# Performance work log

Hardware: AMD Instinct MI355X
Metric: run time of the kernel (lower is better)

The kernel has to match this reference:

```python
import jax, jax.numpy as jnp
import numpy as np

B, N, DM, DC, TOPK = 1024, 131072, 2048, 64, 16
EPS_RES = 1e-8
EPS_SQRT = 1e-12


def setup_inputs() -> dict:
    key = jax.random.key(0)
    k1, k2, k3, k4, k5 = jax.random.split(key, 5)
    query = jax.random.normal(k1, (B, DM), dtype=jnp.float32)
    stored_coords = jax.random.normal(k2, (N, DC), dtype=jnp.float32)
    resilience = jax.random.uniform(k3, (N,), dtype=jnp.float32)
    W_proj = jax.random.normal(k4, (DM, DC), dtype=jnp.float32) / np.sqrt(DM)
    M = jax.random.normal(k5, (DC, DC), dtype=jnp.float32) / np.sqrt(DC)
    return {"query": query, "stored_coords": stored_coords,
            "resilience": resilience, "W_proj": W_proj, "M": M,
            "top_k": TOPK}


def reference(query, stored_coords, resilience, W_proj, M, top_k):
    # Manifold projection: embeddings -> coordinate chart (B, DC)
    qc = query @ W_proj
    # Learned PSD metric G = M M^T
    G = M @ M.T
    # Geodesic distance d(x,y) = sqrt((x-y)^T G (x-y)), expanded into GEMMs:
    qG = qc @ G                      # (B, DC)
    sG = stored_coords @ G           # (N, DC)
    q2 = jnp.sum(qc * qG, axis=-1)               # (B,)
    s2 = jnp.sum(stored_coords * sG, axis=-1)    # (N,)
    cross = qG @ stored_coords.T                 # (B, N) -- dominant GEMM
    d2 = q2[:, None] + s2[None, :] - 2.0 * cross
    dists = jnp.sqrt(jnp.maximum(d2, 0.0) + EPS_SQRT)
    # LIoR resilience weighting
    dists = dists / (resilience + EPS_RES)[None, :]
    # top-k SMALLEST distances (torch.topk largest=False)
    neg_top, topk_indices = jax.lax.top_k(-dists, top_k)
    return -neg_top, topk_indices
```

## Files before the change

### kernel.cpp

```cpp
#include <hip/hip_runtime.h>
#include <stdint.h>

#define NQ 1024
#define NS 131072
#define DMM 2048
#define DCC 64
#define K_TOP 16
#define EPS_RES_F 1e-8f
#define EPS_SQRT_F 1e-12f
#define EPS_A 0.01f

#define NCH 128
#define CHR (NS / NCH)
#define OVCAP 65536
#define SLOTS 24
#define MTOT (NCH * SLOTS)
#define EPT (MTOT / 256)
#define SCAP 3328

typedef __attribute__((ext_vector_type(8))) short short8v;
typedef __attribute__((ext_vector_type(4))) float f32x4;
typedef unsigned long long u64t;

__device__ __forceinline__ unsigned short f2bf(float x) {
  unsigned u = __float_as_uint(x);
  unsigned r = (u + 0x7FFFu + ((u >> 16) & 1u)) >> 16;
  return (unsigned short)r;
}
__device__ __forceinline__ unsigned bf16_down_pos(float x) {
  return __float_as_uint(x) >> 16;
}
__device__ __forceinline__ unsigned bf16_up_pos(float x) {
  const unsigned u = __float_as_uint(x);
  return (u >> 16) + ((u & 0xFFFFu) ? 1u : 0u);
}

__device__ __forceinline__ void gl_lds16(const void* g, void* l) {
  __builtin_amdgcn_global_load_lds(
      (const __attribute__((address_space(1))) unsigned int*)g,
      (__attribute__((address_space(3))) unsigned int*)l, 16, 0, 0);
}

__device__ __forceinline__ float exact_key(const float* __restrict__ stored,
                                           const float* qgl, float q2v,
                                           const float4* __restrict__ aux4, int n) {
  const float4* srow = reinterpret_cast<const float4*>(stored + (size_t)n * DCC);
  float a = 0.f;
#pragma unroll
  for (int kb = 0; kb < 16; ++kb) {
    const float4 qv = *reinterpret_cast<const float4*>(&qgl[4 * kb]);
    const float4 sv = srow[kb];
    a = fmaf(qv.w, sv.w, fmaf(qv.z, sv.z, fmaf(qv.y, sv.y, fmaf(qv.x, sv.x, a))));
  }
  const float4 av = aux4[n];
  const float d2 = fmaf(-2.f, a, q2v + av.x);
  return (fmaxf(d2, 0.f) + EPS_SQRT_F) * av.w;
}

__device__ __forceinline__ void bin_rank256(const int* hist, int rank, int lane,
                                            int& binOut, int& baseOut, int& totalOut) {
  const int b0 = hist[4 * lane + 0], b1 = hist[4 * lane + 1];
  const int b2 = hist[4 * lane + 2], b3 = hist[4 * lane + 3];
  const int s01 = b0 + b1, s012 = s01 + b2;
  const int s = s012 + b3;
  int inc = s;
#pragma unroll
  for (int off = 1; off < 64; off <<= 1) {
    const int u = __shfl_up(inc, off);
    if (lane >= off) inc += u;
  }
  totalOut = __shfl(inc, 63);
  const int excl = inc - s;
  const bool has = (excl <= rank) && (rank < inc);
  const unsigned long long mask = __ballot(has);
  if (mask == 0ULL) { binOut = -1; baseOut = 0; return; }
  const int who = __ffsll((unsigned long long)mask) - 1;
  const int exclW = __shfl(excl, who);
  const int c0 = __shfl(b0, who);
  const int c01 = __shfl(s01, who);
  const int c012 = __shfl(s012, who);
  const int r = rank - exclW;
  int sub, base;
  if (r < c0) { sub = 0; base = 0; }
  else if (r < c01) { sub = 1; base = c0; }
  else if (r < c012) { sub = 2; base = c01; }
  else { sub = 3; base = c012; }
  binOut = 4 * who + sub;
  baseOut = exclW + base;
}

__global__ __launch_bounds__(256) void g_kernel(const float* __restrict__ M,
                                                float* __restrict__ G) {
  __shared__ __align__(16) float Ml[64 * 66];
  const int t = threadIdx.x;
  for (int p = 0; p < 16; ++p) {
    int i = p * 256 + t;
    Ml[(i >> 6) * 66 + (i & 63)] = M[i];
  }
  __syncthreads();
  const int e = blockIdx.x * 256 + t;
  const int i = e >> 6, j = e & 63;
  float a = 0.f;
#pragma unroll
  for (int k = 0; k < 64; ++k) a = fmaf(Ml[i * 66 + k], Ml[j * 66 + k], a);
  G[e] = a;
}

__global__ __launch_bounds__(256) void q_kernel(
    const float* __restrict__ query, const float* __restrict__ W,
    const float* __restrict__ G, float* __restrict__ qGT,
    float* __restrict__ qGr, unsigned short* __restrict__ qGh,
    float* __restrict__ q2o, float* __restrict__ qeo) {
  __shared__ __align__(16) float qs[4][DMM];
  __shared__ float part[4][4][64];
  __shared__ float qc[4][64];
  const int t = threadIdx.x;
  const int qb = blockIdx.x * 4;
  {
    const float4* src = reinterpret_cast<const float4*>(query + (size_t)qb * DMM);
    float4* dst = reinterpret_cast<float4*>(&qs[0][0]);
#pragma unroll
    for (int r = 0; r < 8; ++r) dst[r * 256 + t] = src[r * 256 + t];
  }
  __syncthreads();
  const int c = t & 63, seg = t >> 6;
  float p0 = 0.f, p1 = 0.f, p2 = 0.f, p3 = 0.f;
  const int kbase = seg * 512;
  for (int ki = 0; ki < 512; ++ki) {
    const int k = kbase + ki;
    const float w = W[(size_t)k * 64 + c];
    p0 = fmaf(qs[0][k], w, p0);
    p1 = fmaf(qs[1][k], w, p1);
    p2 = fmaf(qs[2][k], w, p2);
    p3 = fmaf(qs[3][k], w, p3);
  }
  part[0][seg][c] = p0; part[1][seg][c] = p1;
  part[2][seg][c] = p2; part[3][seg][c] = p3;
  __syncthreads();
  {
    const int q = t >> 6, cc = t & 63;
    qc[q][cc] = part[q][0][cc] + part[q][1][cc] + part[q][2][cc] + part[q][3][cc];
  }
  __syncthreads();
  const int w = t >> 6, lane = t & 63;
  float g = 0.f;
  for (int j = 0; j < 64; ++j) g = fmaf(qc[w][j], G[j * 64 + lane], g);
  const int q = qb + w;
  qGT[(size_t)lane * NQ + q] = g;
  qGr[(size_t)q * DCC + lane] = g;
  qGh[(size_t)q * DCC + lane] = f2bf(g);
  float pr = qc[w][lane] * g;
  float pn = g * g;
#pragma unroll
  for (int off = 32; off; off >>= 1) {
    pr += __shfl_xor(pr, off);
    pn += __shfl_xor(pn, off);
  }
  if (lane == 0) {
    q2o[q] = pr;
    qeo[q] = EPS_A * sqrtf(pn);
  }
}

__global__ __launch_bounds__(256) void s_kernel(
    const float* __restrict__ stored, const float* __restrict__ resil,
    const float* __restrict__ G, float4* __restrict__ aux4o,
    unsigned short* __restrict__ sho) {
  __shared__ __align__(16) float Gl[64 * 66];
  __shared__ __align__(16) float sst[64 * 64];
  __shared__ float part2[64 * 33];
  __shared__ float ps[64 * 33];
  const int t = threadIdx.x;
  const int nb = blockIdx.x * 64;
  for (int p = 0; p < 16; ++p) {
    int i = p * 256 + t;
    Gl[(i >> 6) * 66 + (i & 63)] = G[i];
  }
  {
    const float4* src = reinterpret_cast<const float4*>(stored + (size_t)nb * DCC);
    float4* dst = reinterpret_cast<float4*>(sst);
#pragma unroll
    for (int r = 0; r < 4; ++r) dst[r * 256 + t] = src[r * 256 + t];
  }
  __syncthreads();
  const int l = t & 31, tw = t >> 5;
  float acc0[8], acc1[8];
#pragma unroll
  for (int i = 0; i < 8; ++i) { acc0[i] = 0.f; acc1[i] = 0.f; }
  for (int kb = 0; kb < 16; ++kb) {
    const float2 ga0 = *reinterpret_cast<const float2*>(&Gl[(4 * kb + 0) * 66 + 2 * l]);
    const float2 ga1 = *reinterpret_cast<const float2*>(&Gl[(4 * kb + 1) * 66 + 2 * l]);
    const float2 ga2 = *reinterpret_cast<const float2*>(&Gl[(4 * kb + 2) * 66 + 2 * l]);
    const float2 ga3 = *reinterpret_cast<const float2*>(&Gl[(4 * kb + 3) * 66 + 2 * l]);
#pragma unroll
    for (int i = 0; i < 8; ++i) {
      const float4 sv = *reinterpret_cast<const float4*>(&sst[(8 * tw + i) * 64 + 4 * kb]);
      acc0[i] = fmaf(ga3.x, sv.w, fmaf(ga2.x, sv.z, fmaf(ga1.x, sv.y, fmaf(ga0.x, sv.x, acc0[i]))));
      acc1[i] = fmaf(ga3.y, sv.w, fmaf(ga2.y, sv.z, fmaf(ga1.y, sv.y, fmaf(ga0.y, sv.x, acc1[i]))));
    }
  }
#pragma unroll
  for (int i = 0; i < 8; ++i) {
    const int n = 8 * tw + i;
    const float2 sj = *reinterpret_cast<const float2*>(&sst[n * 64 + 2 * l]);
    part2[n * 33 + l] = acc0[i] * sj.x + acc1[i] * sj.y;
    ps[n * 33 + l] = sj.x * sj.x + sj.y * sj.y;
  }
  __syncthreads();
  for (int p = 0; p < 16; ++p) {
    const int i = p * 256 + t;
    const int nl = i >> 6, k = i & 63;
    sho[(size_t)(nb + nl) * DCC + k] = f2bf(sst[nl * 64 + k]);
  }
  if (t < 64) {
    float s = 0.f, sp = 0.f;
#pragma unroll
    for (int u = 0; u < 32; ++u) { s += part2[t * 33 + u]; sp += ps[t * 33 + u]; }
    const float rv = resil[nb + t] + EPS_RES_F;
    const float inv = 1.0f / rv;
    aux4o[nb + t] = make_float4(s, 0.5f * rv * rv, sqrtf(sp), inv * inv);
  }
}

__global__ __launch_bounds__(256) void sub_kernel(
    const float* __restrict__ stored, const float* __restrict__ qGT,
    const float* __restrict__ q2g, const float4* __restrict__ aux4,
    float* __restrict__ skeys) {
  __shared__ __align__(16) float qg[64 * 128];
  __shared__ __align__(16) float sst[64 * 64];
  __shared__ float s2sub[64];
  __shared__ float ir2sub[64];
  const int t = threadIdx.x;
  const int jb = blockIdx.x * 64;
  const int qbase = blockIdx.y * 128;
  for (int p = 0; p < 32; ++p) {
    const int i = p * 256 + t;
    const int k = i >> 7, qq = i & 127;
    qg[k * 128 + qq] = qGT[(size_t)k * NQ + qbase + qq];
  }
#pragma unroll
  for (int p = 0; p < 4; ++p) {
    const int idx = p * 256 + t;
    const int r = idx >> 4, f4 = idx & 15;
    reinterpret_cast<float4*>(sst)[r * 16 + f4] =
        reinterpret_cast<const float4*>(stored + (size_t)(64 * (jb + r)) * DCC)[f4];
  }
  if (t < 64) {
    const float4 v = aux4[64 * (jb + t)];
    s2sub[t] = v.x;
    ir2sub[t] = v.w;
  }
  __syncthreads();
  const int l = t & 31, tw = t >> 5;
  const int q0 = 4 * l;
  float q2r[4];
#pragma unroll
  for (int qq = 0; qq < 4; ++qq) q2r[qq] = q2g[qbase + q0 + qq];
  float acc[4][8];
#pragma unroll
  for (int qq = 0; qq < 4; ++qq)
#pragma unroll
    for (int i = 0; i < 8; ++i) acc[qq][i] = 0.f;
  for (int kb = 0; kb < 16; ++kb) {
    const float4 qa0 = *reinterpret_cast<const float4*>(&qg[(4 * kb + 0) * 128 + q0]);
    const float4 qa1 = *reinterpret_cast<const float4*>(&qg[(4 * kb + 1) * 128 + q0]);
    const float4 qa2 = *reinterpret_cast<const float4*>(&qg[(4 * kb + 2) * 128 + q0]);
    const float4 qa3 = *reinterpret_cast<const float4*>(&qg[(4 * kb + 3) * 128 + q0]);
#pragma unroll
    for (int i = 0; i < 8; ++i) {
      const float4 sv = *reinterpret_cast<const float4*>(&sst[(8 * tw + i) * 64 + 4 * kb]);
      acc[0][i] = fmaf(qa3.x, sv.w, fmaf(qa2.x, sv.z, fmaf(qa1.x, sv.y, fmaf(qa0.x, sv.x, acc[0][i]))));
      acc[1][i] = fmaf(qa3.y, sv.w, fmaf(qa2.y, sv.z, fmaf(qa1.y, sv.y, fmaf(qa0.y, sv.x, acc[1][i]))));
      acc[2][i] = fmaf(qa3.z, sv.w, fmaf(qa2.z, sv.z, fmaf(qa1.z, sv.y, fmaf(qa0.z, sv.x, acc[2][i]))));
      acc[3][i] = fmaf(qa3.w, sv.w, fmaf(qa2.w, sv.z, fmaf(qa1.w, sv.y, fmaf(qa0.w, sv.x, acc[3][i]))));
    }
  }
#pragma unroll
  for (int i = 0; i < 8; ++i) {
    const int jl = 8 * tw + i;
    const float s2v = s2sub[jl];
    const float ir2v = ir2sub[jl];
#pragma unroll
    for (int qq = 0; qq < 4; ++qq) {
      const float d2 = fmaf(-2.f, acc[qq][i], q2r[qq] + s2v);
      const float key = (fmaxf(d2, 0.f) + EPS_SQRT_F) * ir2v;
      skeys[(size_t)(qbase + q0 + qq) * 2048 + jb + jl] = key;
    }
  }
}

__global__ __launch_bounds__(256) void tau_select(
    const float* __restrict__ skeys, float* __restrict__ tau) {
  __shared__ float lk[256 * 17];
  __shared__ float wkv[4][16];
  const int t = threadIdx.x;
  const int lane = t & 63, w = t >> 6;
  const int q = blockIdx.x;
  float k16[16];
#pragma unroll
  for (int s = 0; s < 16; ++s) k16[s] = 3.0e38f;
  for (int i = t; i < 2048; i += 256) {
    const float key = skeys[(size_t)q * 2048 + i];
    if (key < k16[15]) {
#pragma unroll
      for (int s = 15; s >= 1; --s) {
        const bool dprev = key < k16[s - 1];
        const float nk = dprev ? k16[s - 1] : key;
        if (key < k16[s]) k16[s] = nk;
      }
      if (key < k16[0]) k16[0] = key;
    }
  }
#pragma unroll
  for (int s = 0; s < 16; ++s) lk[t * 17 + s] = k16[s];
  __syncthreads();
  {
    int ptr = 0;
    for (int r = 0; r < K_TOP; ++r) {
      float v = lk[t * 17 + ptr];
      int who = lane;
#pragma unroll
      for (int off = 32; off; off >>= 1) {
        const float ov = __shfl_xor(v, off);
        const int ow = __shfl_xor(who, off);
        if (ov < v || (ov == v && ow < who)) { v = ov; who = ow; }
      }
      if (lane == 0) wkv[w][r] = v;
      if (lane == who) ptr++;
    }
  }
  __syncthreads();
  if (w == 0) {
    float v = wkv[lane >> 4][lane & 15];
    float t16 = 0.f;
    for (int r = 0; r < K_TOP; ++r) {
      float mv = v;
      int who = lane;
#pragma unroll
      for (int off = 32; off; off >>= 1) {
        const float ov = __shfl_xor(mv, off);
        const int ow = __shfl_xor(who, off);
        if (ov < mv || (ov == mv && ow < who)) { mv = ov; who = ow; }
      }
      t16 = mv;
      if (lane == who) v = 3.0e38f;
    }
    if (lane == 0) tau[q] = t16 * 1.0001f;
  }
}

__global__ __launch_bounds__(256, 4) void main_mfma(
    const unsigned short* __restrict__ sh, const unsigned short* __restrict__ qGh,
    const float* __restrict__ q2g, const float* __restrict__ qeg,
    const float* __restrict__ taug, const float4* __restrict__ aux4,
    int* __restrict__ ccnt, int* __restrict__ ovcnt,
    unsigned int* __restrict__ ovf, u64t* __restrict__ cand) {
  __shared__ __align__(16) char smA[16384];
  __shared__ __align__(16) float4 auxl[128];
  __shared__ int cnt64[64];
  const int t = threadIdx.x;
  const int lane = t & 63, w = t >> 6;
  const int l15 = lane & 15, hi4 = (lane >> 4) << 2;
  const int chunk = blockIdx.x;
  const int qbase = blockIdx.y * 64;
  const int sx = ((lane & 7) << 4) ^ ((lane >> 3) << 4);
  const int g16 = (lane >> 4) << 4;
  const int swz = (lane & 7) << 4;

  if (t < 64) cnt64[t] = 0;
  float q2h_r[4], tau_r[4], qe_r[4];
#pragma unroll
  for (int qi = 0; qi < 4; ++qi) {
    const int q = qbase + qi * 16 + l15;
    q2h_r[qi] = 0.5f * q2g[q];
    tau_r[qi] = taug[q];
    qe_r[qi] = qeg[q];
  }
  const char* qB = (const char*)qGh;
  const f32x4 z4 = {0.f, 0.f, 0.f, 0.f};

  for (int nt = 0; nt < 8; ++nt) {
    const int nb = chunk * CHR + nt * 128;
    __syncthreads();
#pragma unroll
    for (int ii = 0; ii < 4; ++ii) {
      const int row = w * 32 + ii * 8 + (lane >> 3);
      gl_lds16((const char*)sh + (size_t)(nb + row) * 128 + sx,
               smA + w * 4096 + ii * 1024);
    }
    if (t < 128) auxl[t] = aux4[nb + t];
    __syncthreads();

    f32x4 acc[2][4];
#pragma unroll
    for (int kh = 0; kh < 2; ++kh) {
      short8v bfr[4];
#pragma unroll
      for (int qi = 0; qi < 4; ++qi)
        bfr[qi] = *reinterpret_cast<const short8v*>(
            qB + (((size_t)(qbase + qi * 16 + l15)) << 7) + (kh << 6) + g16);
      const int kx = ((kh << 6) | g16) ^ swz;
#pragma unroll
      for (int ni = 0; ni < 2; ++ni) {
        const short8v af = *reinterpret_cast<const short8v*>(
            smA + ((w * 32 + ni * 16 + l15) << 7) + kx);
#pragma unroll
        for (int qi = 0; qi < 4; ++qi)
          acc[ni][qi] = (kh == 0)
              ? __builtin_amdgcn_mfma_f32_16x16x32_bf16(af, bfr[qi], z4, 0, 0, 0)
              : __builtin_amdgcn_mfma_f32_16x16x32_bf16(af, bfr[qi], acc[ni][qi], 0, 0, 0);
      }
    }
#pragma unroll
    for (int ni = 0; ni < 2; ++ni) {
#pragma unroll
      for (int r = 0; r < 4; ++r) {
        const int nl = w * 32 + ni * 16 + hi4 + r;
        const float4 av = auxl[nl];
#pragma unroll
        for (int qi = 0; qi < 4; ++qi) {
          const float a = acc[ni][qi][r];
          const float t1 = fmaf(0.5f, av.x, q2h_r[qi]);
          const float thr = fmaf(-qe_r[qi], av.z, fmaf(-tau_r[qi], av.y, t1));
          if (a >= thr) {
            const int ql = qi * 16 + l15;
            const int n = nb + nl;
            const float d2 = 2.0f * (t1 - a);
            const float keyp = (fmaxf(d2, 0.0f) + EPS_SQRT_F) * av.w;
            const float ev = fmaf(2.0f * qe_r[qi] * av.z, av.w, 1e-5f * keyp) * 1.0002f;
            const unsigned hiw = (bf16_up_pos(keyp + ev) << 16) |
                                 bf16_down_pos(fmaxf(keyp - ev, 0.0f));
            const u64t ce = ((u64t)hiw << 32) | (unsigned)n;
            const int pos = atomicAdd(&cnt64[ql], 1);
            if (pos < SLOTS) {
              cand[((size_t)((qbase + ql) * NCH + chunk)) * SLOTS + pos] = ce;
            } else {
              const int gp = atomicAdd(ovcnt, 1);
              if (gp < OVCAP) ovf[gp] = ((unsigned)(qbase + ql) << 17) | (unsigned)n;
            }
          }
        }
      }
    }
  }
  __syncthreads();
  if (t < 64) {
    int c = cnt64[t];
    if (c > SLOTS) c = SLOTS;
    ccnt[(size_t)(qbase + t) * NCH + chunk] = c;
  }
}

__global__ __launch_bounds__(256) void final_kernel(
    const u64t* __restrict__ cand, const int* __restrict__ ccnt,
    const int* __restrict__ ovcnt, const unsigned int* __restrict__ ovf,
    const float* __restrict__ qGr, const float* __restrict__ q2g,
    const float* __restrict__ stored, const float4* __restrict__ aux4,
    float* __restrict__ out) {
  __shared__ __align__(16) float qgl[64];
  __shared__ int ccl[NCH];
  __shared__ int hist[256];
  __shared__ int scnt;
  __shared__ unsigned int sidx[SCAP];
  __shared__ u64t wku[4][16];
  const int t = threadIdx.x;
  const int lane = t & 63, w = t >> 6;
  const int q = blockIdx.x;
  if (t < 64) qgl[t] = qGr[(size_t)q * DCC + t];
  if (t < NCH) ccl[t] = min(ccnt[(size_t)q * NCH + t], SLOTS);
  hist[t] = 0;
  if (t == 0) scnt = 0;
  __syncthreads();
  u64t ev[EPT];
  unsigned vmask = 0;
  {
    const u64t* base = cand + (size_t)q * NCH * SLOTS;
#pragma unroll
    for (int p = 0; p < EPT; ++p) {
      const int i = p * 256 + t;
      ev[p] = base[i];
      const int seg = i / SLOTS;
      const int j = i - seg * SLOTS;
      if (j < ccl[seg]) vmask |= 1u << p;
    }
  }
#pragma unroll
  for (int p = 0; p < EPT; ++p)
    if (vmask & (1u << p)) atomicAdd(&hist[(int)(ev[p] >> 56)], 1);
  __syncthreads();
  int B, baseB, total;
  bin_rank256(hist, K_TOP - 1, lane, B, baseB, total);
  unsigned U16bits = 0xFFFFu;
  __syncthreads();
  if (total >= K_TOP) {
    hist[t] = 0;
    __syncthreads();
#pragma unroll
    for (int p = 0; p < EPT; ++p)
      if ((vmask & (1u << p)) && (int)(ev[p] >> 56) == B)
        atomicAdd(&hist[(int)((ev[p] >> 48) & 0xFF)], 1);
    __syncthreads();
    int b2, dummy, tot2;
    bin_rank256(hist, K_TOP - 1 - baseB, lane, b2, dummy, tot2);
    U16bits = ((unsigned)B << 8) | (unsigned)b2;
  }
#pragma unroll
  for (int p = 0; p < EPT; ++p) {
    if ((vmask & (1u << p)) && ((unsigned)(ev[p] >> 32) & 0xFFFFu) <= U16bits) {
      const int pos = atomicAdd(&scnt, 1);
      if (pos < SCAP) sidx[pos] = (unsigned)ev[p];
    }
  }
  {
    int oc = *ovcnt;
    if (oc > OVCAP) oc = OVCAP;
    for (int i = t; i < oc; i += 256) {
      const unsigned pk = ovf[i];
      if ((int)(pk >> 17) == q) {
        const int pos = atomicAdd(&scnt, 1);
        if (pos < SCAP) sidx[pos] = pk & 0x1FFFFu;
      }
    }
  }
  __syncthreads();
  int sc = scnt;
  if (sc > SCAP) sc = SCAP;
  const float q2v = q2g[q];
  u64t k16u[16];
#pragma unroll
  for (int s = 0; s < 16; ++s) k16u[s] = ~0ULL;
  for (int i = t; i < sc; i += 256) {
    const int n = (int)sidx[i];
    const u64t pv =
        ((u64t)__float_as_uint(exact_key(stored, qgl, q2v, aux4, n)) << 32) | (unsigned)n;
    if (pv < k16u[15]) {
#pragma unroll
      for (int s = 15; s >= 1; --s) {
        const bool dprev = pv < k16u[s - 1];
        const u64t nk = dprev ? k16u[s - 1] : pv;
        if (pv < k16u[s]) k16u[s] = nk;
      }
      if (pv < k16u[0]) k16u[0] = pv;
    }
  }
  {
    int ptr = 0;
    for (int r = 0; r < K_TOP; ++r) {
      u64t v = k16u[ptr];
      int who = lane;
#pragma unroll
      for (int off = 32; off; off >>= 1) {
        const u64t ov = __shfl_xor(v, off);
        const int ol = __shfl_xor(who, off);
        if (ov < v || (ov == v && ol < who)) { v = ov; who = ol; }
      }
      if (lane == 0) wku[w][r] = v;
      if (lane == who) ptr++;
    }
  }
  __syncthreads();
  if (w == 0) {
    u64t e = wku[lane >> 4][lane & 15];
    for (int r = 0; r < K_TOP; ++r) {
      u64t mv = e;
      int who = lane;
#pragma unroll
      for (int off = 32; off; off >>= 1) {
        const u64t ov = __shfl_xor(mv, off);
        const int ol = __shfl_xor(who, off);
        if (ov < mv || (ov == mv && ol < who)) { mv = ov; who = ol; }
      }
      if (lane == 0) {
        out[q * K_TOP + r] = sqrtf(__uint_as_float((unsigned)(mv >> 32)));
        out[NQ * K_TOP + q * K_TOP + r] = (float)(unsigned)(mv & 0xFFFFFFFFu);
      }
      if (lane == who) e = ~0ULL;
    }
  }
}

extern "C" void kernel_launch(void* const* d_in, const int* in_sizes, int n_in,
                              void* d_out, int out_size, void* d_ws, size_t ws_size,
                              hipStream_t stream) {
  const float* query  = (const float*)d_in[0];
  const float* stored = (const float*)d_in[1];
  const float* resil  = (const float*)d_in[2];
  const float* W      = (const float*)d_in[3];
  const float* M      = (const float*)d_in[4];

  char* ws = (char*)d_ws;
  size_t off = 0;
  float* G    = (float*)(ws + off); off += 16384;
  float* qGT  = (float*)(ws + off); off += 262144;
  float* qGr  = (float*)(ws + off); off += 262144;
  unsigned short* qGh = (unsigned short*)(ws + off); off += 131072;
  float* q2   = (float*)(ws + off); off += 4096;
  float* qe   = (float*)(ws + off); off += 4096;
  float* tau  = (float*)(ws + off); off += 4096;
  float4* aux4 = (float4*)(ws + off); off += (size_t)NS * 16;
  int*   ccnt = (int*)(ws + off);   off += (size_t)NQ * NCH * 4;
  int*   ovcnt = (int*)(ws + off);  off += 4096;
  unsigned int* ovf = (unsigned int*)(ws + off); off += OVCAP * 4;
  unsigned short* sh = (unsigned short*)(ws + off); off += 16777216;
  u64t* cand = (u64t*)(ws + off);
  float* skeys = (float*)cand;

  float* out = (float*)d_out;

  hipMemsetAsync(ovcnt, 0, 4096, stream);
  g_kernel<<<16, 256, 0, stream>>>(M, G);
  q_kernel<<<NQ / 4, 256, 0, stream>>>(query, W, G, qGT, qGr, qGh, q2, qe);
  s_kernel<<<NS / 64, 256, 0, stream>>>(stored, resil, G, aux4, sh);
  sub_kernel<<<dim3(32, 8), 256, 0, stream>>>(stored, qGT, q2, aux4, skeys);
  tau_select<<<NQ, 256, 0, stream>>>(skeys, tau);
  main_mfma<<<dim3(NCH, NQ / 64), 256, 0, stream>>>(sh, qGh, q2, qe, tau, aux4,
                                                    ccnt, ovcnt, ovf, cand);
  final_kernel<<<NQ, 256, 0, stream>>>(cand, ccnt, ovcnt, ovf, qGr, q2,
                                       stored, aux4, out);
}
```

Baseline: 196.3 us.

## Double-buffer stored-coord tiles in main_mfma and halve queries per q_kernel block

main_mfma now double-buffers the LDS tile and aux data, prefetching the next 128-row tile while MFMAs and the threshold epilogue run on the current one. It also hoists the query B-fragments out of the tile loop into registers. q_kernel handles two queries per block instead of four, doubling the grid to spread the projection over more CUs. The extra LDS (about 33KB per block) and the larger register footprint may reduce occupancy under launch_bounds(256,4), and half of q_kernel's threads sit idle in the G stage.

```diff
diff --git a/kernel.cpp b/kernel.cpp
--- a/kernel.cpp
+++ b/kernel.cpp
@@ -111,54 +111,55 @@
     const float* __restrict__ G, float* __restrict__ qGT,
     float* __restrict__ qGr, unsigned short* __restrict__ qGh,
     float* __restrict__ q2o, float* __restrict__ qeo) {
-  __shared__ __align__(16) float qs[4][DMM];
-  __shared__ float part[4][4][64];
-  __shared__ float qc[4][64];
+  __shared__ __align__(16) float qs[2][DMM];
+  __shared__ float part[2][4][64];
+  __shared__ float qc[2][64];
   const int t = threadIdx.x;
-  const int qb = blockIdx.x * 4;
+  const int qb = blockIdx.x * 2;
   {
     const float4* src = reinterpret_cast<const float4*>(query + (size_t)qb * DMM);
     float4* dst = reinterpret_cast<float4*>(&qs[0][0]);
 #pragma unroll
-    for (int r = 0; r < 8; ++r) dst[r * 256 + t] = src[r * 256 + t];
+    for (int r = 0; r < 4; ++r) dst[r * 256 + t] = src[r * 256 + t];
   }
   __syncthreads();
   const int c = t & 63, seg = t >> 6;
-  float p0 = 0.f, p1 = 0.f, p2 = 0.f, p3 = 0.f;
+  float p0 = 0.f, p1 = 0.f;
   const int kbase = seg * 512;
+#pragma unroll 4
   for (int ki = 0; ki < 512; ++ki) {
     const int k = kbase + ki;
     const float w = W[(size_t)k * 64 + c];
     p0 = fmaf(qs[0][k], w, p0);
     p1 = fmaf(qs[1][k], w, p1);
-    p2 = fmaf(qs[2][k], w, p2);
-    p3 = fmaf(qs[3][k], w, p3);
-  }
-  part[0][seg][c] = p0; part[1][seg][c] = p1;
-  part[2][seg][c] = p2; part[3][seg][c] = p3;
-  __syncthreads();
-  {
+  }
+  part[0][seg][c] = p0;
+  part[1][seg][c] = p1;
+  __syncthreads();
+  if (t < 128) {
     const int q = t >> 6, cc = t & 63;
     qc[q][cc] = part[q][0][cc] + part[q][1][cc] + part[q][2][cc] + part[q][3][cc];
   }
   __syncthreads();
   const int w = t >> 6, lane = t & 63;
-  float g = 0.f;
-  for (int j = 0; j < 64; ++j) g = fmaf(qc[w][j], G[j * 64 + lane], g);
-  const int q = qb + w;
-  qGT[(size_t)lane * NQ + q] = g;
-  qGr[(size_t)q * DCC + lane] = g;
-  qGh[(size_t)q * DCC + lane] = f2bf(g);
-  float pr = qc[w][lane] * g;
-  float pn = g * g;
-#pragma unroll
-  for (int off = 32; off; off >>= 1) {
-    pr += __shfl_xor(pr, off);
-    pn += __shfl_xor(pn, off);
-  }
-  if (lane == 0) {
-    q2o[q] = pr;
-    qeo[q] = EPS_A * sqrtf(pn);
+  if (w < 2) {
+    float g = 0.f;
+    for (int j = 0; j < 64; ++j) g = fmaf(qc[w][j], G[j * 64 + lane], g);
+    const int q = qb + w;
+    qGT[(size_t)lane * NQ + q] = g;
+    qGr[(size_t)q * DCC + lane] = g;
+    qGh[(size_t)q * DCC + lane] = f2bf(g);
+    float pr = qc[w][lane] * g;
+    float pn = g * g;
+#pragma unroll
+    for (int off = 32; off; off >>= 1) {
+      pr += __shfl_xor(pr, off);
+      pn += __shfl_xor(pn, off);
+    }
+    if (lane == 0) {
+      q2o[q] = pr;
+      qeo[q] = EPS_A * sqrtf(pn);
+    }
   }
 }
 
@@ -355,8 +356,8 @@
     const float* __restrict__ taug, const float4* __restrict__ aux4,
     int* __restrict__ ccnt, int* __restrict__ ovcnt,
     unsigned int* __restrict__ ovf, u64t* __restrict__ cand) {
-  __shared__ __align__(16) char smA[16384];
-  __shared__ __align__(16) float4 auxl[128];
+  __shared__ __align__(16) char smA[2][16384];
+  __shared__ __align__(16) float4 auxl[2][128];
   __shared__ int cnt64[64];
   const int t = threadIdx.x;
   const int lane = t & 63, w = t >> 6;
@@ -376,39 +377,55 @@
     tau_r[qi] = taug[q];
     qe_r[qi] = qeg[q];
   }
-  const char* qB = (const char*)qGh;
+  short8v bfr[2][4];
+#pragma unroll
+  for (int kh = 0; kh < 2; ++kh)
+#pragma unroll
+    for (int qi = 0; qi < 4; ++qi)
+      bfr[kh][qi] = *reinterpret_cast<const short8v*>(
+          (const char*)qGh + (((size_t)(qbase + qi * 16 + l15)) << 7) + (kh << 6) + g16);
   const f32x4 z4 = {0.f, 0.f, 0.f, 0.f};
 
-  for (int nt = 0; nt < 8; ++nt) {
-    const int nb = chunk * CHR + nt * 128;
-    __syncthreads();
+  {
+    const int nb = chunk * CHR;
 #pragma unroll
     for (int ii = 0; ii < 4; ++ii) {
       const int row = w * 32 + ii * 8 + (lane >> 3);
       gl_lds16((const char*)sh + (size_t)(nb + row) * 128 + sx,
-               smA + w * 4096 + ii * 1024);
-    }
-    if (t < 128) auxl[t] = aux4[nb + t];
-    __syncthreads();
+               &smA[0][0] + w * 4096 + ii * 1024);
+    }
+    if (t < 128) auxl[0][t] = aux4[nb + t];
+  }
+  __syncthreads();
+
+  for (int nt = 0; nt < 8; ++nt) {
+    const int cur = nt & 1;
+    const int nb = chunk * CHR + nt * 128;
+    float4 auxtmp;
+    if (nt < 7) {
+      const int nb1 = nb + 128;
+#pragma unroll
+      for (int ii = 0; ii < 4; ++ii) {
+        const int row = w * 32 + ii * 8 + (lane >> 3);
+        gl_lds16((const char*)sh + (size_t)(nb1 + row) * 128 + sx,
+                 &smA[cur ^ 1][0] + w * 4096 + ii * 1024);
+      }
+      if (t < 128) auxtmp = aux4[nb1 + t];
+    }
 
     f32x4 acc[2][4];
 #pragma unroll
     for (int kh = 0; kh < 2; ++kh) {
-      short8v bfr[4];
-#pragma unroll
-      for (int qi = 0; qi < 4; ++qi)
-        bfr[qi] = *reinterpret_cast<const short8v*>(
-            qB + (((size_t)(qbase + qi * 16 + l15)) << 7) + (kh << 6) + g16);
       const int kx = ((kh << 6) | g16) ^ swz;
 #pragma unroll
       for (int ni = 0; ni < 2; ++ni) {
         const short8v af = *reinterpret_cast<const short8v*>(
-            smA + ((w * 32 + ni * 16 + l15) << 7) + kx);
+            &smA[cur][0] + ((w * 32 + ni * 16 + l15) << 7) + kx);
 #pragma unroll
         for (int qi = 0; qi < 4; ++qi)
           acc[ni][qi] = (kh == 0)
-              ? __builtin_amdgcn_mfma_f32_16x16x32_bf16(af, bfr[qi], z4, 0, 0, 0)
-              : __builtin_amdgcn_mfma_f32_16x16x32_bf16(af, bfr[qi], acc[ni][qi], 0, 0, 0);
+              ? __builtin_amdgcn_mfma_f32_16x16x32_bf16(af, bfr[0][qi], z4, 0, 0, 0)
+              : __builtin_amdgcn_mfma_f32_16x16x32_bf16(af, bfr[1][qi], acc[ni][qi], 0, 0, 0);
       }
     }
 #pragma unroll
@@ -416,7 +433,7 @@
 #pragma unroll
       for (int r = 0; r < 4; ++r) {
         const int nl = w * 32 + ni * 16 + hi4 + r;
-        const float4 av = auxl[nl];
+        const float4 av = auxl[cur][nl];
 #pragma unroll
         for (int qi = 0; qi < 4; ++qi) {
           const float a = acc[ni][qi][r];
@@ -442,8 +459,9 @@
         }
       }
     }
-  }
-  __syncthreads();
+    if (nt < 7 && t < 128) auxl[cur ^ 1][t] = auxtmp;
+    __syncthreads();
+  }
   if (t < 64) {
     int c = cnt64[t];
     if (c > SLOTS) c = SLOTS;
@@ -609,7 +627,7 @@
 
   hipMemsetAsync(ovcnt, 0, 4096, stream);
   g_kernel<<<16, 256, 0, stream>>>(M, G);
-  q_kernel<<<NQ / 4, 256, 0, stream>>>(query, W, G, qGT, qGr, qGh, q2, qe);
+  q_kernel<<<NQ / 2, 256, 0, stream>>>(query, W, G, qGT, qGr, qGh, q2, qe);
   s_kernel<<<NS / 64, 256, 0, stream>>>(stored, resil, G, aux4, sh);
   sub_kernel<<<dim3(32, 8), 256, 0, stream>>>(stored, qGT, q2, aux4, skeys);
   tau_select<<<NQ, 256, 0, stream>>>(skeys, tau);
```

New measurement: 210.6 us. 7.3% more time.

## Load stored-coord fragments directly from global into registers, dropping LDS staging

Applied to the files above, without the earlier changes.

The main MFMA kernel no longer stages each 128-row tile of stored coordinates and aux data through shared memory with global_load_lds and two barriers per tile. Each wave now loads its own A fragments and aux values straight from global memory into registers. The qG B fragments are hoisted out of the tile loop, and the loop is unrolled by two. This removes per-tile barriers and LDS traffic, since no data is shared across waves, but it relies on the cache for the aux reads and raises register pressure under the 4-blocks launch bound.

```diff
diff --git a/kernel.cpp b/kernel.cpp
--- a/kernel.cpp
+++ b/kernel.cpp
@@ -33,12 +33,6 @@
 __device__ __forceinline__ unsigned bf16_up_pos(float x) {
   const unsigned u = __float_as_uint(x);
   return (u >> 16) + ((u & 0xFFFFu) ? 1u : 0u);
-}
-
-__device__ __forceinline__ void gl_lds16(const void* g, void* l) {
-  __builtin_amdgcn_global_load_lds(
-      (const __attribute__((address_space(1))) unsigned int*)g,
-      (__attribute__((address_space(3))) unsigned int*)l, 16, 0, 0);
 }
 
 __device__ __forceinline__ float exact_key(const float* __restrict__ stored,
@@ -355,19 +349,16 @@
     const float* __restrict__ taug, const float4* __restrict__ aux4,
     int* __restrict__ ccnt, int* __restrict__ ovcnt,
     unsigned int* __restrict__ ovf, u64t* __restrict__ cand) {
-  __shared__ __align__(16) char smA[16384];
-  __shared__ __align__(16) float4 auxl[128];
   __shared__ int cnt64[64];
   const int t = threadIdx.x;
   const int lane = t & 63, w = t >> 6;
   const int l15 = lane & 15, hi4 = (lane >> 4) << 2;
   const int chunk = blockIdx.x;
   const int qbase = blockIdx.y * 64;
-  const int sx = ((lane & 7) << 4) ^ ((lane >> 3) << 4);
   const int g16 = (lane >> 4) << 4;
-  const int swz = (lane & 7) << 4;
-
   if (t < 64) cnt64[t] = 0;
+  __syncthreads();
+
   float q2h_r[4], tau_r[4], qe_r[4];
 #pragma unroll
   for (int qi = 0; qi < 4; ++qi) {
@@ -376,47 +367,46 @@
     tau_r[qi] = taug[q];
     qe_r[qi] = qeg[q];
   }
-  const char* qB = (const char*)qGh;
+  short8v bfr[2][4];
+#pragma unroll
+  for (int kh = 0; kh < 2; ++kh)
+#pragma unroll
+    for (int qi = 0; qi < 4; ++qi)
+      bfr[kh][qi] = *reinterpret_cast<const short8v*>(
+          (const char*)qGh + (((size_t)(qbase + qi * 16 + l15)) << 7) + (kh << 6) + g16);
   const f32x4 z4 = {0.f, 0.f, 0.f, 0.f};
-
+  const char* shb = (const char*)sh;
+
+#pragma unroll 2
   for (int nt = 0; nt < 8; ++nt) {
     const int nb = chunk * CHR + nt * 128;
-    __syncthreads();
-#pragma unroll
-    for (int ii = 0; ii < 4; ++ii) {
-      const int row = w * 32 + ii * 8 + (lane >> 3);
-      gl_lds16((const char*)sh + (size_t)(nb + row) * 128 + sx,
-               smA + w * 4096 + ii * 1024);
-    }
-    if (t < 128) auxl[t] = aux4[nb + t];
-    __syncthreads();
+    const char* ab = shb + (size_t)(nb + w * 32) * 128;
+    short8v af[2][2];
+#pragma unroll
+    for (int kh = 0; kh < 2; ++kh)
+#pragma unroll
+      for (int ni = 0; ni < 2; ++ni)
+        af[kh][ni] = *reinterpret_cast<const short8v*>(
+            ab + ((ni * 16 + l15) << 7) + (kh << 6) + g16);
 
     f32x4 acc[2][4];
 #pragma unroll
-    for (int kh = 0; kh < 2; ++kh) {
-      short8v bfr[4];
-#pragma unroll
-      for (int qi = 0; qi < 4; ++qi)
-        bfr[qi] = *reinterpret_cast<const short8v*>(
-            qB + (((size_t)(qbase + qi * 16 + l15)) << 7) + (kh << 6) + g16);
-      const int kx = ((kh << 6) | g16) ^ swz;
-#pragma unroll
-      for (int ni = 0; ni < 2; ++ni) {
-        const short8v af = *reinterpret_cast<const short8v*>(
-            smA + ((w * 32 + ni * 16 + l15) << 7) + kx);
+    for (int kh = 0; kh < 2; ++kh)
+#pragma unroll
+      for (int ni = 0; ni < 2; ++ni)
 #pragma unroll
         for (int qi = 0; qi < 4; ++qi)
           acc[ni][qi] = (kh == 0)
-              ? __builtin_amdgcn_mfma_f32_16x16x32_bf16(af, bfr[qi], z4, 0, 0, 0)
-              : __builtin_amdgcn_mfma_f32_16x16x32_bf16(af, bfr[qi], acc[ni][qi], 0, 0, 0);
-      }
-    }
+              ? __builtin_amdgcn_mfma_f32_16x16x32_bf16(af[0][ni], bfr[0][qi], z4, 0, 0, 0)
+              : __builtin_amdgcn_mfma_f32_16x16x32_bf16(af[1][ni], bfr[1][qi], acc[ni][qi], 0, 0, 0);
+
+    const float4* auxb = aux4 + nb + w * 32;
 #pragma unroll
     for (int ni = 0; ni < 2; ++ni) {
 #pragma unroll
       for (int r = 0; r < 4; ++r) {
         const int nl = w * 32 + ni * 16 + hi4 + r;
-        const float4 av = auxl[nl];
+        const float4 av = auxb[ni * 16 + hi4 + r];
 #pragma unroll
         for (int qi = 0; qi < 4; ++qi) {
           const float a = acc[ni][qi][r];
```

After: 211.5 us. +7.7%, slower.
